# Optimization experiments

Hardware: AMD Instinct MI355X
Metric: run time of the kernel (lower is better)

Reference implementation:

```python
import jax, jax.numpy as jnp
import numpy as np

B, L, D, H = 4, 4096, 1024, 16
HD = D // H  # head_dim = 64
SCALE = 1.0 / np.sqrt(HD)


def setup_inputs() -> dict:
    key = jax.random.key(0)
    ks = jax.random.split(key, 6)
    x = jax.random.normal(ks[0], (B, L, D), dtype=jnp.float32)
    Wqkv_w = jax.random.normal(ks[1], (3 * D, D), dtype=jnp.float32) * (1.0 / np.sqrt(D))
    Wqkv_b = jax.random.normal(ks[2], (3 * D,), dtype=jnp.float32) * 0.02
    out_w = jax.random.normal(ks[3], (D, D), dtype=jnp.float32) * (1.0 / np.sqrt(D))
    out_b = jax.random.normal(ks[4], (D,), dtype=jnp.float32) * 0.02
    gamma_raw = jax.random.uniform(ks[5], (H,), dtype=jnp.float32, minval=0.0, maxval=2.0)
    return {"x": x, "Wqkv_w": Wqkv_w, "Wqkv_b": Wqkv_b,
            "out_w": out_w, "out_b": out_b, "gamma_raw": gamma_raw}


def reference(x, Wqkv_w, Wqkv_b, out_w, out_b, gamma_raw):
    b, l, dm = x.shape
    # qkv projection: [B, L, 3*D] -> [3, B, H, L, hd]
    qkv = x @ Wqkv_w.T + Wqkv_b
    qkv = qkv.reshape(b, l, 3, H, HD).transpose(2, 0, 3, 1, 4)
    q, k, v = qkv[0], qkv[1], qkv[2]      # each [B, H, L, hd]
    k = k * SCALE
    g = jax.nn.sigmoid(gamma_raw)          # [H]
    gb = g[None, :, None, None]            # broadcast over [B, H, hd, hd]

    # move time axis to front for scan: [L, B, H, hd]
    qT = q.transpose(2, 0, 1, 3)
    kT = k.transpose(2, 0, 1, 3)
    vT = v.transpose(2, 0, 1, 3)

    def step(state, qkv_t):
        q_t, k_t, v_t = qkv_t
        # S = gamma * S + v k^T
        state = gb * state + jnp.einsum('bhi,bhj->bhij', v_t, k_t)
        # y = S q
        y_t = jnp.einsum('bhij,bhj->bhi', state, q_t)
        return state, y_t

    state0 = jnp.zeros((b, H, HD, HD), dtype=x.dtype)
    _, y = jax.lax.scan(step, state0, (qT, kT, vT))  # y: [L, B, H, hd]

    y = y.transpose(1, 0, 2, 3).reshape(b, l, dm)    # [B, L, D]
    return y @ out_w.T + out_b
```

## Files before the change

### kernel.cpp

```cpp
#include <hip/hip_runtime.h>
#include <cstdint>
#include <cstddef>

#define B_    4
#define L_    4096
#define D_    1024
#define H_    16
#define HD_   64
#define ND3_  3072
#define M1_   16384
#define NCH_  64
#define CSZ_  64
#define SCALE_ 0.125f

typedef __attribute__((ext_vector_type(8))) __bf16 bf16x8;
typedef __attribute__((ext_vector_type(4))) float f32x4;
typedef __attribute__((ext_vector_type(4))) unsigned int uint4v;

__device__ __forceinline__ float u2f(unsigned int u) { return __builtin_bit_cast(float, u); }
__device__ __forceinline__ unsigned int f2u(float f) { return __builtin_bit_cast(unsigned int, f); }
__device__ __forceinline__ float bf2f(unsigned short s) { return u2f(((unsigned int)s) << 16); }
__device__ __forceinline__ unsigned short f2bf(float f) {
  unsigned int u = f2u(f);
  u = u + 0x7fffu + ((u >> 16) & 1u);
  return (unsigned short)(u >> 16);
}

__device__ __forceinline__ void glds16(const unsigned short* g, unsigned short* l) {
  __builtin_amdgcn_global_load_lds(
      (const __attribute__((address_space(1))) void*)(uintptr_t)g,
      (__attribute__((address_space(3))) void*)(uintptr_t)l, 16, 0, 0);
}

__global__ __launch_bounds__(256) void cast_kernel(const float* __restrict__ in,
                                                   unsigned short* __restrict__ out, int n)
{
  int i = (blockIdx.x * 256 + threadIdx.x) * 4;
  if (i + 3 < n) {
    float4 f = *(const float4*)(in + i);
    out[i + 0] = f2bf(f.x);
    out[i + 1] = f2bf(f.y);
    out[i + 2] = f2bf(f.z);
    out[i + 3] = f2bf(f.w);
  }
}

__global__ __launch_bounds__(512, 2)
void gemm_qkv8(const unsigned short* __restrict__ A, const unsigned short* __restrict__ Bm,
               const float* __restrict__ bias,
               unsigned short* __restrict__ qo, unsigned short* __restrict__ ko,
               unsigned short* __restrict__ vo, int M, int N, int K)
{
  __shared__ __align__(16) unsigned short Ab[2 * 2 * 8192];
  __shared__ __align__(16) unsigned short Bb[2 * 2 * 8192];

  const int nwg = gridDim.x;
  const int wg = (blockIdx.x & 7) * (nwg >> 3) + (blockIdx.x >> 3);
  const int nbn = N >> 8;
  const int bm = wg / nbn, bn = wg - bm * nbn;
  const int m0 = bm << 8, n0 = bn << 8;
  const int tid = threadIdx.x;
  const int lane = tid & 63, wid = tid >> 6;
  const int wr = wid >> 2, wc = wid & 3;
  const int fl = lane & 15, fh = lane >> 4;
  const int swz = fl & 7;

  const int nt = K >> 6;

  const int srow = lane >> 3;
  const int slc = (lane & 7) ^ srow;

  f32x4 acc[2][2][4][2] = {};

  auto stage = [&](const unsigned short* Mat, int rbase, int h, int kt,
                   unsigned short* buf) {
    const int d = kt & 1;
#pragma unroll
    for (int s = 0; s < 2; ++s) {
      const int rl = (wid * 2 + s) * 8 + srow;
      glds16(Mat + (size_t)(rbase + h * 128 + rl) * K + kt * 64 + slc * 8,
             buf + (d * 2 + h) * 8192 + (wid * 2 + s) * 512);
    }
  };

  stage(A, m0, 0, 0, Ab); stage(Bm, n0, 0, 0, Bb);
  stage(A, m0, 1, 0, Ab); stage(Bm, n0, 1, 0, Bb);
  stage(Bm, n0, 0, 1, Bb); stage(A, m0, 0, 1, Ab);
  asm volatile("s_waitcnt vmcnt(4)" ::: "memory");
  __builtin_amdgcn_s_barrier();
  __builtin_amdgcn_sched_barrier(0);

  for (int t = 0; t < nt; ++t) {
    const int d = t & 1;
    const unsigned short* Abuf = Ab + d * 16384;
    const unsigned short* Bbuf = Bb + d * 16384;
    bf16x8 af0[4][2], af1[4][2], bf0[2][2], bf1[2][2];

#pragma unroll
    for (int m = 0; m < 4; ++m)
#pragma unroll
      for (int ks = 0; ks < 2; ++ks)
        af0[m][ks] = *(const bf16x8*)(Abuf + (wr * 64 + m * 16 + fl) * 64 + ((ks * 4 + fh) ^ swz) * 8);
#pragma unroll
    for (int n = 0; n < 2; ++n)
#pragma unroll
      for (int ks = 0; ks < 2; ++ks)
        bf0[n][ks] = *(const bf16x8*)(Bbuf + (wc * 32 + n * 16 + fl) * 64 + ((ks * 4 + fh) ^ swz) * 8);
    if (t + 1 < nt) stage(A, m0, 1, t + 1, Ab);
    __builtin_amdgcn_s_barrier();
    asm volatile("s_waitcnt lgkmcnt(0)" ::: "memory");
    __builtin_amdgcn_sched_barrier(0);
    __builtin_amdgcn_s_setprio(1);
#pragma unroll
    for (int m = 0; m < 4; ++m)
#pragma unroll
      for (int n = 0; n < 2; ++n)
#pragma unroll
        for (int ks = 0; ks < 2; ++ks)
          acc[0][0][m][n] = __builtin_amdgcn_mfma_f32_16x16x32_bf16(af0[m][ks], bf0[n][ks], acc[0][0][m][n], 0, 0, 0);
    __builtin_amdgcn_s_setprio(0);
    __builtin_amdgcn_s_barrier();

#pragma unroll
    for (int m = 0; m < 4; ++m)
#pragma unroll
      for (int ks = 0; ks < 2; ++ks)
        af1[m][ks] = *(const bf16x8*)(Abuf + 8192 + (wr * 64 + m * 16 + fl) * 64 + ((ks * 4 + fh) ^ swz) * 8);
    if (t + 1 < nt) stage(Bm, n0, 1, t + 1, Bb);
    __builtin_amdgcn_s_barrier();
    asm volatile("s_waitcnt lgkmcnt(0)" ::: "memory");
    __builtin_amdgcn_sched_barrier(0);
    __builtin_amdgcn_s_setprio(1);
#pragma unroll
    for (int m = 0; m < 4; ++m)
#pragma unroll
      for (int n = 0; n < 2; ++n)
#pragma unroll
        for (int ks = 0; ks < 2; ++ks)
          acc[1][0][m][n] = __builtin_amdgcn_mfma_f32_16x16x32_bf16(af1[m][ks], bf0[n][ks], acc[1][0][m][n], 0, 0, 0);
    __builtin_amdgcn_s_setprio(0);
    __builtin_amdgcn_s_barrier();

#pragma unroll
    for (int n = 0; n < 2; ++n)
#pragma unroll
      for (int ks = 0; ks < 2; ++ks)
        bf1[n][ks] = *(const bf16x8*)(Bbuf + 8192 + (wc * 32 + n * 16 + fl) * 64 + ((ks * 4 + fh) ^ swz) * 8);
    if (t + 2 < nt) stage(Bm, n0, 0, t + 2, Bb);
    __builtin_amdgcn_s_barrier();
    asm volatile("s_waitcnt lgkmcnt(0)" ::: "memory");
    __builtin_amdgcn_sched_barrier(0);
    __builtin_amdgcn_s_setprio(1);
#pragma unroll
    for (int m = 0; m < 4; ++m)
#pragma unroll
      for (int n = 0; n < 2; ++n)
#pragma unroll
        for (int ks = 0; ks < 2; ++ks)
          acc[0][1][m][n] = __builtin_amdgcn_mfma_f32_16x16x32_bf16(af0[m][ks], bf1[n][ks], acc[0][1][m][n], 0, 0, 0);
    __builtin_amdgcn_s_setprio(0);
    __builtin_amdgcn_s_barrier();

    if (t + 2 < nt) stage(A, m0, 0, t + 2, Ab);
    __builtin_amdgcn_s_setprio(1);
#pragma unroll
    for (int m = 0; m < 4; ++m)
#pragma unroll
      for (int n = 0; n < 2; ++n)
#pragma unroll
        for (int ks = 0; ks < 2; ++ks)
          acc[1][1][m][n] = __builtin_amdgcn_mfma_f32_16x16x32_bf16(af1[m][ks], bf1[n][ks], acc[1][1][m][n], 0, 0, 0);
    __builtin_amdgcn_s_setprio(0);
    if (t < nt - 2) { asm volatile("s_waitcnt vmcnt(4)" ::: "memory"); }
    else            { asm volatile("s_waitcnt vmcnt(0)" ::: "memory"); }
    __builtin_amdgcn_s_barrier();
    __builtin_amdgcn_sched_barrier(0);
  }

  const int rb = fh << 2;
#pragma unroll
  for (int mh = 0; mh < 2; ++mh) {
#pragma unroll
    for (int nh = 0; nh < 2; ++nh) {
#pragma unroll
      for (int m = 0; m < 4; ++m) {
#pragma unroll
        for (int n = 0; n < 2; ++n) {
#pragma unroll
          for (int r = 0; r < 4; ++r) {
            int row = m0 + mh * 128 + wr * 64 + m * 16 + rb + r;
            int col = n0 + nh * 128 + wc * 32 + n * 16 + fl;
            float val = acc[mh][nh][m][n][r] + bias[col];
            int which = col >> 10;
            int hh = (col >> 6) & 15;
            int hd = col & 63;
            int bb = row >> 12;
            int tt2 = row & 4095;
            size_t idx = (((size_t)(bb * H_ + hh)) * L_ + tt2) * HD_ + hd;
            if (which == 0)      qo[idx] = f2bf(val);
            else if (which == 1) ko[idx] = f2bf(val * SCALE_);
            else                 vo[idx] = f2bf(val);
          }
        }
      }
    }
  }
}

__global__ __launch_bounds__(256, 3)
void gemm_out(const unsigned short* __restrict__ A, const unsigned short* __restrict__ Bm,
              const float* __restrict__ bias, float* __restrict__ Co, int M, int N, int K)
{
  constexpr int BM = 128, BN = 128, WM = 2, WN = 2;
  constexpr int TR = 64;
  constexpr int AR = BM / TR;
  constexpr int FM = BM / WM / 16;
  constexpr int FN = BN / WN / 16;
  constexpr int ASZ = BM * 32, BSZ = BN * 32;

  __shared__ __align__(16) unsigned short Ab[3 * ASZ];
  __shared__ __align__(16) unsigned short Bb[3 * BSZ];

  const int nwg = gridDim.x;
  const int wg = (blockIdx.x & 7) * (nwg >> 3) + (blockIdx.x >> 3);
  const int nbn = N / BN;
  const int bm = wg / nbn, bn = wg - bm * nbn;
  const int m0 = bm * BM, n0 = bn * BN;
  const int tid = threadIdx.x;
  const int lane = tid & 63, wid = tid >> 6;
  const int wr = wid / WN, wc = wid % WN;
  const int fl = lane & 15, fh = lane >> 4;

  const int rowbase = wid * 16 + (lane >> 2);
  const int ckst = (lane & 3) ^ ((rowbase & 3) ^ ((rowbase >> 2) & 3));
  const int ckrd = fh ^ ((fl & 3) ^ ((fl >> 2) & 3));

  const int nt = K >> 5;

  f32x4 acc[FM][FN] = {};

  auto stageA = [&](int kt, int d) {
#pragma unroll
    for (int s = 0; s < AR; ++s)
      glds16(A + (size_t)(m0 + s * TR + rowbase) * K + kt * 32 + ckst * 8,
             Ab + d * ASZ + s * TR * 32 + wid * 512);
  };
  auto stageB = [&](int kt, int d) {
#pragma unroll
    for (int s = 0; s < AR; ++s)
      glds16(Bm + (size_t)(n0 + s * TR + rowbase) * K + kt * 32 + ckst * 8,
             Bb + d * BSZ + s * TR * 32 + wid * 512);
  };

  stageA(0, 0); stageB(0, 0);
  stageA(1, 1); stageB(1, 1);

  for (int t = 0; t < nt; ++t) {
    const int d = t % 3;
    if (t < nt - 1) { asm volatile("s_waitcnt vmcnt(4)" ::: "memory"); }
    else            { asm volatile("s_waitcnt vmcnt(0)" ::: "memory"); }
    __builtin_amdgcn_s_barrier();
    __builtin_amdgcn_sched_barrier(0);

    const unsigned short* Abuf = Ab + d * ASZ;
    const unsigned short* Bbuf = Bb + d * BSZ;

    bf16x8 bfrag[FN], afrag[FM / 2];
#pragma unroll
    for (int n = 0; n < FN; ++n)
      bfrag[n] = *(const bf16x8*)(Bbuf + (wc * (BN / WN) + n * 16 + fl) * 32 + ckrd * 8);
#pragma unroll
    for (int m = 0; m < FM / 2; ++m)
      afrag[m] = *(const bf16x8*)(Abuf + (wr * (BM / WM) + m * 16 + fl) * 32 + ckrd * 8);
    if (t + 2 < nt) stageA(t + 2, (t + 2) % 3);
    asm volatile("s_waitcnt lgkmcnt(0)" ::: "memory");
    __builtin_amdgcn_sched_barrier(0);
    __builtin_amdgcn_s_setprio(1);
#pragma unroll
    for (int m = 0; m < FM / 2; ++m)
#pragma unroll
      for (int n = 0; n < FN; ++n)
        acc[m][n] = __builtin_amdgcn_mfma_f32_16x16x32_bf16(afrag[m], bfrag[n], acc[m][n], 0, 0, 0);
    __builtin_amdgcn_s_setprio(0);

    bf16x8 afrag2[FM / 2];
#pragma unroll
    for (int m = 0; m < FM / 2; ++m)
      afrag2[m] = *(const bf16x8*)(Abuf + (wr * (BM / WM) + (m + FM / 2) * 16 + fl) * 32 + ckrd * 8);
    if (t + 2 < nt) stageB(t + 2, (t + 2) % 3);
    asm volatile("s_waitcnt lgkmcnt(0)" ::: "memory");
    __builtin_amdgcn_sched_barrier(0);
    __builtin_amdgcn_s_setprio(1);
#pragma unroll
    for (int m = 0; m < FM / 2; ++m)
#pragma unroll
      for (int n = 0; n < FN; ++n)
        acc[m + FM / 2][n] = __builtin_amdgcn_mfma_f32_16x16x32_bf16(afrag2[m], bfrag[n], acc[m + FM / 2][n], 0, 0, 0);
    __builtin_amdgcn_s_setprio(0);
  }

  const int rb = fh << 2;
#pragma unroll
  for (int m = 0; m < FM; ++m)
#pragma unroll
    for (int n = 0; n < FN; ++n)
#pragma unroll
      for (int r = 0; r < 4; ++r) {
        int row = m0 + wr * (BM / WM) + m * 16 + rb + r;
        int col = n0 + wc * (BN / WN) + n * 16 + fl;
        Co[(size_t)row * N + col] = acc[m][n][r] + bias[col];
      }
}

__global__ __launch_bounds__(256) void ret_phase1(
    const unsigned short* __restrict__ kb, const unsigned short* __restrict__ vb,
    const float* __restrict__ gamma_raw, unsigned short* __restrict__ Sbuf)
{
  int bhc = blockIdx.x;
  int c = bhc & 63, bh = bhc >> 6, h = bh & 15;
  float g = 1.f / (1.f + expf(-gamma_raw[h]));
  float lg2g = log2f(g);

  __shared__ __align__(16) unsigned short Kt[64][72];
  __shared__ __align__(16) unsigned short Vwt[64][72];

  int tid = threadIdx.x;
  size_t base = ((size_t)bh * L_ + (size_t)c * CSZ_) * HD_;
#pragma unroll
  for (int qq = 0; qq < 16; ++qq) {
    int e = tid + qq * 256;
    int j = e >> 6, col = e & 63;
    float wj = exp2f(lg2g * (float)(63 - j));
    Kt[col][j] = kb[base + e];
    Vwt[col][j] = f2bf(bf2f(vb[base + e]) * wj);
  }
  __syncthreads();

  int lane = tid & 63, w = tid >> 6;
  int fl = lane & 15, fh = lane >> 4;

  bf16x8 av0 = *(const bf16x8*)(&Vwt[w * 16 + fl][fh * 8]);
  bf16x8 av1 = *(const bf16x8*)(&Vwt[w * 16 + fl][32 + fh * 8]);

  int rb = fh << 2;
  unsigned short* out = Sbuf + (size_t)bhc * 4096;
#pragma unroll
  for (int jf = 0; jf < 4; ++jf) {
    bf16x8 bk0 = *(const bf16x8*)(&Kt[jf * 16 + fl][fh * 8]);
    bf16x8 bk1 = *(const bf16x8*)(&Kt[jf * 16 + fl][32 + fh * 8]);
    f32x4 z = {};
    z = __builtin_amdgcn_mfma_f32_16x16x32_bf16(av0, bk0, z, 0, 0, 0);
    z = __builtin_amdgcn_mfma_f32_16x16x32_bf16(av1, bk1, z, 0, 0, 0);
#pragma unroll
    for (int r = 0; r < 4; ++r) {
      int a = w * 16 + rb + r, bcol = jf * 16 + fl;
      out[a * 64 + bcol] = f2bf(z[r]);
    }
  }
}

__global__ __launch_bounds__(256) void ret_phase2(unsigned short* __restrict__ Sbuf,
                                                  const float* __restrict__ gamma_raw)
{
  int bh = blockIdx.x >> 3, grp = blockIdx.x & 7;
  int h = bh & 15;
  float g = 1.f / (1.f + expf(-gamma_raw[h]));
  float gC = powf(g, 64.f);
  int e = (grp * 256 + threadIdx.x) * 2;
  unsigned short* base = Sbuf + (size_t)bh * (NCH_ * 4096) + e;
  float s0 = 0.f, s1 = 0.f;
  for (int c = 0; c < NCH_; ++c) {
    unsigned int u = *(unsigned int*)(base + (size_t)c * 4096);
    float a0 = bf2f((unsigned short)(u & 0xffffu));
    float a1 = bf2f((unsigned short)(u >> 16));
    *(unsigned int*)(base + (size_t)c * 4096) =
        (unsigned int)f2bf(s0) | ((unsigned int)f2bf(s1) << 16);
    s0 = gC * s0 + a0;
    s1 = gC * s1 + a1;
  }
}

__global__ __launch_bounds__(256) void ret_phase3(
    const unsigned short* __restrict__ qb, const unsigned short* __restrict__ kb,
    const unsigned short* __restrict__ vb, const unsigned short* __restrict__ Sbuf,
    const float* __restrict__ gamma_raw, unsigned short* __restrict__ y)
{
  int bhc = blockIdx.x;
  int c = bhc & 63, bh = bhc >> 6, h = bh & 15, b = bh >> 4;
  float g = 1.f / (1.f + expf(-gamma_raw[h]));
  float lg2g = log2f(g);

  __shared__ __align__(16) unsigned short Qs[64][72];
  __shared__ __align__(16) unsigned short Ks[64][72];
  __shared__ __align__(16) unsigned short Vt[64][72];
  __shared__ __align__(16) unsigned short Sb[64][72];
  __shared__ __align__(16) unsigned short Ps[64][72];

  int tid = threadIdx.x;
  size_t base = ((size_t)bh * L_ + (size_t)c * CSZ_) * HD_;
  const unsigned short* Sp = Sbuf + (size_t)bhc * 4096;
#pragma unroll
  for (int qq = 0; qq < 16; ++qq) {
    int e = tid + qq * 256;
    int r = e >> 6, col = e & 63;
    Qs[r][col] = qb[base + e];
    Ks[r][col] = kb[base + e];
    Vt[col][r] = vb[base + e];
    Sb[r][col] = Sp[e];
  }
  __syncthreads();

  int lane = tid & 63, w = tid >> 6;
  int fl = lane & 15, fh = lane >> 4;
  int rb = fh << 2;

  bf16x8 aq0 = *(const bf16x8*)(&Qs[w * 16 + fl][fh * 8]);
  bf16x8 aq1 = *(const bf16x8*)(&Qs[w * 16 + fl][32 + fh * 8]);

  f32x4 pc[4], acc[4];
#pragma unroll
  for (int jf = 0; jf < 4; ++jf) {
    bf16x8 bk0 = *(const bf16x8*)(&Ks[jf * 16 + fl][fh * 8]);
    bf16x8 bk1 = *(const bf16x8*)(&Ks[jf * 16 + fl][32 + fh * 8]);
    f32x4 z = {};
    z = __builtin_amdgcn_mfma_f32_16x16x32_bf16(aq0, bk0, z, 0, 0, 0);
    z = __builtin_amdgcn_mfma_f32_16x16x32_bf16(aq1, bk1, z, 0, 0, 0);
    pc[jf] = z;

    bf16x8 bs0 = *(const bf16x8*)(&Sb[jf * 16 + fl][fh * 8]);
    bf16x8 bs1 = *(const bf16x8*)(&Sb[jf * 16 + fl][32 + fh * 8]);
    f32x4 zz = {};
    zz = __builtin_amdgcn_mfma_f32_16x16x32_bf16(aq0, bs0, zz, 0, 0, 0);
    zz = __builtin_amdgcn_mfma_f32_16x16x32_bf16(aq1, bs1, zz, 0, 0, 0);
    acc[jf] = zz;
  }

#pragma unroll
  for (int jf = 0; jf < 4; ++jf) {
#pragma unroll
    for (int r = 0; r < 4; ++r) {
      int i = w * 16 + rb + r, j = jf * 16 + fl;
      float val = (j <= i) ? pc[jf][r] * exp2f(lg2g * (float)(i - j)) : 0.f;
      Ps[i][j] = f2bf(val);
    }
  }

  float gi1[4];
#pragma unroll
  for (int r = 0; r < 4; ++r) gi1[r] = exp2f(lg2g * (float)(w * 16 + rb + r + 1));
#pragma unroll
  for (int jf = 0; jf < 4; ++jf)
#pragma unroll
    for (int r = 0; r < 4; ++r) acc[jf][r] *= gi1[r];

  __syncthreads();

  bf16x8 ap0 = *(const bf16x8*)(&Ps[w * 16 + fl][fh * 8]);
  bf16x8 ap1 = *(const bf16x8*)(&Ps[w * 16 + fl][32 + fh * 8]);
#pragma unroll
  for (int jf = 0; jf < 4; ++jf) {
    bf16x8 bv0 = *(const bf16x8*)(&Vt[jf * 16 + fl][fh * 8]);
    bf16x8 bv1 = *(const bf16x8*)(&Vt[jf * 16 + fl][32 + fh * 8]);
    acc[jf] = __builtin_amdgcn_mfma_f32_16x16x32_bf16(ap0, bv0, acc[jf], 0, 0, 0);
    acc[jf] = __builtin_amdgcn_mfma_f32_16x16x32_bf16(ap1, bv1, acc[jf], 0, 0, 0);
  }

  size_t yrow = ((size_t)(b * L_ + c * CSZ_)) * D_ + h * HD_;
#pragma unroll
  for (int jf = 0; jf < 4; ++jf) {
#pragma unroll
    for (int r = 0; r < 4; ++r) {
      int i = w * 16 + rb + r;
      y[yrow + (size_t)i * D_ + jf * 16 + fl] = f2bf(acc[jf][r]);
    }
  }
}

extern "C" void kernel_launch(void* const* d_in, const int* in_sizes, int n_in,
                              void* d_out, int out_size, void* d_ws, size_t ws_size,
                              hipStream_t stream)
{
  const float* x        = (const float*)d_in[0];
  const float* Wqkv_w   = (const float*)d_in[1];
  const float* Wqkv_b   = (const float*)d_in[2];
  const float* out_w    = (const float*)d_in[3];
  const float* out_b    = (const float*)d_in[4];
  const float* gamma_raw= (const float*)d_in[5];
  float* out = (float*)d_out;

  char* ws = (char*)d_ws;
  unsigned short* x_bf    = (unsigned short*)ws; ws += (size_t)16777216 * 2;
  unsigned short* wqkv_bf = (unsigned short*)ws; ws += (size_t)3145728 * 2;
  unsigned short* wout_bf = (unsigned short*)ws; ws += (size_t)1048576 * 2;
  unsigned short* qb      = (unsigned short*)ws; ws += (size_t)16777216 * 2;
  unsigned short* kb      = (unsigned short*)ws; ws += (size_t)16777216 * 2;
  unsigned short* vb      = (unsigned short*)ws; ws += (size_t)16777216 * 2;
  unsigned short* Sbuf    = (unsigned short*)ws; ws += (size_t)16777216 * 2;
  unsigned short* yb      = (unsigned short*)ws; ws += (size_t)16777216 * 2;

  cast_kernel<<<16384, 256, 0, stream>>>(x, x_bf, 16777216);
  cast_kernel<<<3072, 256, 0, stream>>>(Wqkv_w, wqkv_bf, 3145728);
  cast_kernel<<<1024, 256, 0, stream>>>(out_w, wout_bf, 1048576);

  gemm_qkv8<<<64 * 12, 512, 0, stream>>>(x_bf, wqkv_bf, Wqkv_b,
                                         qb, kb, vb, M1_, ND3_, D_);

  ret_phase1<<<4096, 256, 0, stream>>>(kb, vb, gamma_raw, Sbuf);
  ret_phase2<<<512, 256, 0, stream>>>(Sbuf, gamma_raw);
  ret_phase3<<<4096, 256, 0, stream>>>(qb, kb, vb, Sbuf, gamma_raw, yb);

  gemm_out<<<128 * 8, 256, 0, stream>>>(yb, wout_bf, out_b, out, M1_, D_, D_);
}
```

Baseline: 242.6 us.

## Merge cast launches and reuse 256x256 gemm8 kernel for output projection

The three fp32-to-bf16 cast launches become one kernel that picks its source by block index, which saves launch overhead. The output projection now runs on the templated 256x256-tile, 512-thread QKV GEMM kernel with a plain row-major fp32 epilogue, replacing the separate 128x128 gemm_out kernel. Larger tiles give more data reuse per workgroup, but the output GEMM launches only 256 workgroups, which may underfill the device's CUs.

Result: faster. 233.3 us (-3.8%).

```diff
diff --git a/kernel.cpp b/kernel.cpp
--- a/kernel.cpp
+++ b/kernel.cpp
@@ -32,24 +32,30 @@
       (__attribute__((address_space(3))) void*)(uintptr_t)l, 16, 0, 0);
 }
 
-__global__ __launch_bounds__(256) void cast_kernel(const float* __restrict__ in,
-                                                   unsigned short* __restrict__ out, int n)
-{
-  int i = (blockIdx.x * 256 + threadIdx.x) * 4;
-  if (i + 3 < n) {
-    float4 f = *(const float4*)(in + i);
-    out[i + 0] = f2bf(f.x);
-    out[i + 1] = f2bf(f.y);
-    out[i + 2] = f2bf(f.z);
-    out[i + 3] = f2bf(f.w);
-  }
-}
-
+__global__ __launch_bounds__(256) void cast3_kernel(
+    const float* __restrict__ x, unsigned short* __restrict__ xo,
+    const float* __restrict__ w1, unsigned short* __restrict__ w1o,
+    const float* __restrict__ w2, unsigned short* __restrict__ w2o)
+{
+  const float* in; unsigned short* out; int i;
+  int blk = blockIdx.x;
+  if (blk < 16384)      { in = x;  out = xo;  i = (blk * 256 + threadIdx.x) * 4; }
+  else if (blk < 19456) { in = w1; out = w1o; i = ((blk - 16384) * 256 + threadIdx.x) * 4; }
+  else                  { in = w2; out = w2o; i = ((blk - 19456) * 256 + threadIdx.x) * 4; }
+  float4 f = *(const float4*)(in + i);
+  out[i + 0] = f2bf(f.x);
+  out[i + 1] = f2bf(f.y);
+  out[i + 2] = f2bf(f.z);
+  out[i + 3] = f2bf(f.w);
+}
+
+template<int EPI>
 __global__ __launch_bounds__(512, 2)
-void gemm_qkv8(const unsigned short* __restrict__ A, const unsigned short* __restrict__ Bm,
-               const float* __restrict__ bias,
-               unsigned short* __restrict__ qo, unsigned short* __restrict__ ko,
-               unsigned short* __restrict__ vo, int M, int N, int K)
+void gemm8(const unsigned short* __restrict__ A, const unsigned short* __restrict__ Bm,
+           const float* __restrict__ bias,
+           unsigned short* __restrict__ qo, unsigned short* __restrict__ ko,
+           unsigned short* __restrict__ vo, float* __restrict__ Co,
+           int M, int N, int K)
 {
   __shared__ __align__(16) unsigned short Ab[2 * 2 * 8192];
   __shared__ __align__(16) unsigned short Bb[2 * 2 * 8192];
@@ -191,125 +197,24 @@
             int row = m0 + mh * 128 + wr * 64 + m * 16 + rb + r;
             int col = n0 + nh * 128 + wc * 32 + n * 16 + fl;
             float val = acc[mh][nh][m][n][r] + bias[col];
-            int which = col >> 10;
-            int hh = (col >> 6) & 15;
-            int hd = col & 63;
-            int bb = row >> 12;
-            int tt2 = row & 4095;
-            size_t idx = (((size_t)(bb * H_ + hh)) * L_ + tt2) * HD_ + hd;
-            if (which == 0)      qo[idx] = f2bf(val);
-            else if (which == 1) ko[idx] = f2bf(val * SCALE_);
-            else                 vo[idx] = f2bf(val);
+            if constexpr (EPI == 0) {
+              int which = col >> 10;
+              int hh = (col >> 6) & 15;
+              int hd = col & 63;
+              int bb = row >> 12;
+              int tt2 = row & 4095;
+              size_t idx = (((size_t)(bb * H_ + hh)) * L_ + tt2) * HD_ + hd;
+              if (which == 0)      qo[idx] = f2bf(val);
+              else if (which == 1) ko[idx] = f2bf(val * SCALE_);
+              else                 vo[idx] = f2bf(val);
+            } else {
+              Co[(size_t)row * N + col] = val;
+            }
           }
         }
       }
     }
   }
-}
-
-__global__ __launch_bounds__(256, 3)
-void gemm_out(const unsigned short* __restrict__ A, const unsigned short* __restrict__ Bm,
-              const float* __restrict__ bias, float* __restrict__ Co, int M, int N, int K)
-{
-  constexpr int BM = 128, BN = 128, WM = 2, WN = 2;
-  constexpr int TR = 64;
-  constexpr int AR = BM / TR;
-  constexpr int FM = BM / WM / 16;
-  constexpr int FN = BN / WN / 16;
-  constexpr int ASZ = BM * 32, BSZ = BN * 32;
-
-  __shared__ __align__(16) unsigned short Ab[3 * ASZ];
-  __shared__ __align__(16) unsigned short Bb[3 * BSZ];
-
-  const int nwg = gridDim.x;
-  const int wg = (blockIdx.x & 7) * (nwg >> 3) + (blockIdx.x >> 3);
-  const int nbn = N / BN;
-  const int bm = wg / nbn, bn = wg - bm * nbn;
-  const int m0 = bm * BM, n0 = bn * BN;
-  const int tid = threadIdx.x;
-  const int lane = tid & 63, wid = tid >> 6;
-  const int wr = wid / WN, wc = wid % WN;
-  const int fl = lane & 15, fh = lane >> 4;
-
-  const int rowbase = wid * 16 + (lane >> 2);
-  const int ckst = (lane & 3) ^ ((rowbase & 3) ^ ((rowbase >> 2) & 3));
-  const int ckrd = fh ^ ((fl & 3) ^ ((fl >> 2) & 3));
-
-  const int nt = K >> 5;
-
-  f32x4 acc[FM][FN] = {};
-
-  auto stageA = [&](int kt, int d) {
-#pragma unroll
-    for (int s = 0; s < AR; ++s)
-      glds16(A + (size_t)(m0 + s * TR + rowbase) * K + kt * 32 + ckst * 8,
-             Ab + d * ASZ + s * TR * 32 + wid * 512);
-  };
-  auto stageB = [&](int kt, int d) {
-#pragma unroll
-    for (int s = 0; s < AR; ++s)
-      glds16(Bm + (size_t)(n0 + s * TR + rowbase) * K + kt * 32 + ckst * 8,
-             Bb + d * BSZ + s * TR * 32 + wid * 512);
-  };
-
-  stageA(0, 0); stageB(0, 0);
-  stageA(1, 1); stageB(1, 1);
-
-  for (int t = 0; t < nt; ++t) {
-    const int d = t % 3;
-    if (t < nt - 1) { asm volatile("s_waitcnt vmcnt(4)" ::: "memory"); }
-    else            { asm volatile("s_waitcnt vmcnt(0)" ::: "memory"); }
-    __builtin_amdgcn_s_barrier();
-    __builtin_amdgcn_sched_barrier(0);
-
-    const unsigned short* Abuf = Ab + d * ASZ;
-    const unsigned short* Bbuf = Bb + d * BSZ;
-
-    bf16x8 bfrag[FN], afrag[FM / 2];
-#pragma unroll
-    for (int n = 0; n < FN; ++n)
-      bfrag[n] = *(const bf16x8*)(Bbuf + (wc * (BN / WN) + n * 16 + fl) * 32 + ckrd * 8);
-#pragma unroll
-    for (int m = 0; m < FM / 2; ++m)
-      afrag[m] = *(const bf16x8*)(Abuf + (wr * (BM / WM) + m * 16 + fl) * 32 + ckrd * 8);
-    if (t + 2 < nt) stageA(t + 2, (t + 2) % 3);
-    asm volatile("s_waitcnt lgkmcnt(0)" ::: "memory");
-    __builtin_amdgcn_sched_barrier(0);
-    __builtin_amdgcn_s_setprio(1);
-#pragma unroll
-    for (int m = 0; m < FM / 2; ++m)
-#pragma unroll
-      for (int n = 0; n < FN; ++n)
-        acc[m][n] = __builtin_amdgcn_mfma_f32_16x16x32_bf16(afrag[m], bfrag[n], acc[m][n], 0, 0, 0);
-    __builtin_amdgcn_s_setprio(0);
-
-    bf16x8 afrag2[FM / 2];
-#pragma unroll
-    for (int m = 0; m < FM / 2; ++m)
-      afrag2[m] = *(const bf16x8*)(Abuf + (wr * (BM / WM) + (m + FM / 2) * 16 + fl) * 32 + ckrd * 8);
-    if (t + 2 < nt) stageB(t + 2, (t + 2) % 3);
-    asm volatile("s_waitcnt lgkmcnt(0)" ::: "memory");
-    __builtin_amdgcn_sched_barrier(0);
-    __builtin_amdgcn_s_setprio(1);
-#pragma unroll
-    for (int m = 0; m < FM / 2; ++m)
-#pragma unroll
-      for (int n = 0; n < FN; ++n)
-        acc[m + FM / 2][n] = __builtin_amdgcn_mfma_f32_16x16x32_bf16(afrag2[m], bfrag[n], acc[m + FM / 2][n], 0, 0, 0);
-    __builtin_amdgcn_s_setprio(0);
-  }
-
-  const int rb = fh << 2;
-#pragma unroll
-  for (int m = 0; m < FM; ++m)
-#pragma unroll
-    for (int n = 0; n < FN; ++n)
-#pragma unroll
-      for (int r = 0; r < 4; ++r) {
-        int row = m0 + wr * (BM / WM) + m * 16 + rb + r;
-        int col = n0 + wc * (BN / WN) + n * 16 + fl;
-        Co[(size_t)row * N + col] = acc[m][n][r] + bias[col];
-      }
 }
 
 __global__ __launch_bounds__(256) void ret_phase1(
@@ -498,16 +403,15 @@
   unsigned short* Sbuf    = (unsigned short*)ws; ws += (size_t)16777216 * 2;
   unsigned short* yb      = (unsigned short*)ws; ws += (size_t)16777216 * 2;
 
-  cast_kernel<<<16384, 256, 0, stream>>>(x, x_bf, 16777216);
-  cast_kernel<<<3072, 256, 0, stream>>>(Wqkv_w, wqkv_bf, 3145728);
-  cast_kernel<<<1024, 256, 0, stream>>>(out_w, wout_bf, 1048576);
-
-  gemm_qkv8<<<64 * 12, 512, 0, stream>>>(x_bf, wqkv_bf, Wqkv_b,
-                                         qb, kb, vb, M1_, ND3_, D_);
+  cast3_kernel<<<20480, 256, 0, stream>>>(x, x_bf, Wqkv_w, wqkv_bf, out_w, wout_bf);
+
+  gemm8<0><<<64 * 12, 512, 0, stream>>>(x_bf, wqkv_bf, Wqkv_b,
+                                        qb, kb, vb, nullptr, M1_, ND3_, D_);
 
   ret_phase1<<<4096, 256, 0, stream>>>(kb, vb, gamma_raw, Sbuf);
   ret_phase2<<<512, 256, 0, stream>>>(Sbuf, gamma_raw);
   ret_phase3<<<4096, 256, 0, stream>>>(qb, kb, vb, Sbuf, gamma_raw, yb);
 
-  gemm_out<<<128 * 8, 256, 0, stream>>>(yb, wout_bf, out_b, out, M1_, D_, D_);
-}
+  gemm8<1><<<64 * 4, 512, 0, stream>>>(yb, wout_bf, out_b,
+                                       nullptr, nullptr, nullptr, out, M1_, D_, D_);
+}
```
